# Performance work log

Hardware: AMD Instinct MI355X
Metric: run time of the kernel (lower is better)

The kernel has to match this reference:

```python
import jax, jax.numpy as jnp
import numpy as np

DIM = 128      # matrix dimension of the positional maps
N = 1024       # number of unique tree positions
MAX_POS = 65536  # positions < 2^16 -> path length <= 15 bits
L = 16         # static number of scan steps (covers max path length)


def setup_inputs() -> dict:
    key = jax.random.key(0)
    k1, k2 = jax.random.split(key)
    # replicate torch init: rand(2,d,d).softmax(-1).cumsum(-1)
    u = jax.random.uniform(k1, (2, DIM, DIM), dtype=jnp.float32)
    primitives = jnp.cumsum(jax.nn.softmax(u, axis=-1), axis=-1)
    unique = jax.random.randint(k2, (N,), 0, MAX_POS, dtype=jnp.int64)
    return {"unique": unique, "primitives": primitives}


def reference(unique, primitives):
    dtype = primitives.dtype
    dim = primitives.shape[-1]
    # hermitian = P - P^H (real -> skew-symmetric); primitives = matrix_exp(hermitian)
    herm = primitives - jnp.swapaxes(primitives, -1, -2)          # [2, d, d]
    expP = jax.vmap(jax.scipy.linalg.expm)(herm)                  # [2, d, d]
    eye = jnp.eye(dim, dtype=dtype)
    # linear(x, W) = x @ W.T ; word==2 (padding / exhausted path) applies identity
    trans = jnp.stack([expP[0].T, expP[1].T, eye])                # [3, d, d]

    # pos_to_path: bits of pos, LSB-first, dropping the leading 1.
    # bit at step s is (pos >> s) & 1, valid while (pos >> s) >= 2; pos<=1 -> empty path.
    steps = jnp.arange(L, dtype=unique.dtype)
    shifted = unique[None, :] >> steps[:, None]                   # [L, N]
    words = jnp.where(shifted >= 2, shifted & 1, 2)               # [L, N] in {0,1,2}

    def step(maps, w):
        # maps[n] <- maps[n] @ trans[w[n]]   (sequential composition along the path)
        return jnp.einsum('nij,njk->nik', maps, trans[w]), None

    maps0 = jnp.broadcast_to(eye, (unique.shape[0], dim, dim))    # identity.repeat(N,1,1)
    maps, _ = jax.lax.scan(step, maps0, words)
    return maps
```

## Files before the change

kernel.cpp:

```cpp
#include <hip/hip_runtime.h>

typedef unsigned int uint32;
typedef unsigned short u16;
typedef __attribute__((ext_vector_type(8))) short bf16x8;
typedef __attribute__((ext_vector_type(4))) float f32x4;
typedef __attribute__((ext_vector_type(2))) uint32 u32x2;
typedef __attribute__((ext_vector_type(4))) uint32 u32x4;

#define DIM 128
#define MAT (DIM * DIM)
#define GR  2048
#define PLANE 16384
#define MFMA __builtin_amdgcn_mfma_f32_16x16x32_bf16


__device__ __forceinline__ u16 f2bf(float x) {
    uint32 u = __float_as_uint(x);
    u += 0x7fffu + ((u >> 16) & 1u);
    return (u16)(u >> 16);
}
__device__ __forceinline__ float bf2f(u16 h) { return __uint_as_float(((uint32)h) << 16); }
__device__ __forceinline__ void split2(float x, u16& a0, u16& a1) {
    a0 = f2bf(x); a1 = f2bf(x - bf2f(a0));
}
__device__ __forceinline__ uint32 pack2(u16 a, u16 b) { return (uint32)a | ((uint32)b << 16); }
__device__ __forceinline__ uint4 packu4(const u16 (&a)[8]) {
    uint4 v; v.x = pack2(a[0], a[1]); v.y = pack2(a[2], a[3]);
    v.z = pack2(a[4], a[5]); v.w = pack2(a[6], a[7]); return v;
}
__device__ __forceinline__ uint32 comp4(const uint4& v, int c) {
    return c == 0 ? v.x : c == 1 ? v.y : c == 2 ? v.z : v.w;
}
__device__ __forceinline__ void transp8(const uint4 (&in)[8], uint4 (&out)[8]) {
#pragma unroll
    for (int c = 0; c < 8; ++c) {
        u16 o[8];
#pragma unroll
        for (int k = 0; k < 8; ++k) o[k] = (u16)(comp4(in[k], c >> 1) >> ((c & 1) * 16));
        out[c].x = pack2(o[0], o[1]); out[c].y = pack2(o[2], o[3]);
        out[c].z = pack2(o[4], o[5]); out[c].w = pack2(o[6], o[7]);
    }
}

template<bool PBLDS, int NP>
__device__ __forceinline__ void mm2(const uint4* __restrict__ pah, const uint4* __restrict__ pal,
                                    const uint4* __restrict__ pbh, const uint4* __restrict__ pbl,
                                    f32x4 (&acc)[4][4]) {
    const int tid = threadIdx.x, lane = tid & 63, w = tid >> 6;
    const int wr = (w >> 1) * 64, wc = (w & 1) * 64, lr = lane & 15, lg = lane >> 4;
#pragma unroll 1
    for (int kb = 0; kb < 4; ++kb) {
        const int g = kb * 4 + lg;
        bf16x8 ah[4], al[4], bh[4], bl[4];
#pragma unroll
        for (int t = 0; t < 4; ++t) {
            int ra = wr + t * 16 + lr;
            ah[t] = *(const bf16x8*)&pah[g * 128 + ra];
            if (NP == 3) al[t] = *(const bf16x8*)&pal[g * 128 + ra];
            int rb = wc + t * 16 + lr;
            int ib = PBLDS ? (rb * 16 + (g ^ (rb & 7))) : (g * 128 + rb);
            bh[t] = *(const bf16x8*)&pbh[ib];
            if (NP == 3) bl[t] = *(const bf16x8*)&pbl[ib];
        }
#pragma unroll
        for (int i = 0; i < 4; ++i)
#pragma unroll
            for (int j = 0; j < 4; ++j) {
                acc[i][j] = MFMA(ah[i], bh[j], acc[i][j], 0, 0, 0);
                if (NP == 3) {
                    acc[i][j] = MFMA(ah[i], bl[j], acc[i][j], 0, 0, 0);
                    acc[i][j] = MFMA(al[i], bh[j], acc[i][j], 0, 0, 0);
                }
            }
    }
}

__device__ __forceinline__ void acc_to_lds2(const f32x4 (&acc)[4][4], uint4* Mh, uint4* Ml) {
    const int tid = threadIdx.x, lane = tid & 63, w = tid >> 6;
    const int wr = (w >> 1) * 64, wc = (w & 1) * 64, lr = lane & 15, lg = lane >> 4;
#pragma unroll
    for (int i = 0; i < 4; ++i) {
        int u0 = wr + i * 16 + 4 * lg, half = (u0 >> 2) & 1, gq = u0 >> 3;
#pragma unroll
        for (int j = 0; j < 4; ++j) {
            int m = wc + j * 16 + lr;
            u16 h[4], l[4];
#pragma unroll
            for (int q = 0; q < 4; ++q) split2(acc[i][j][q], h[q], l[q]);
            uint2 hv; hv.x = pack2(h[0], h[1]); hv.y = pack2(h[2], h[3]);
            uint2 lv; lv.x = pack2(l[0], l[1]); lv.y = pack2(l[2], l[3]);
            int base = m * 16 + (gq ^ (m & 7));
            ((uint2*)&Mh[base])[half] = hv;
            ((uint2*)&Ml[base])[half] = lv;
        }
    }
}

__device__ __forceinline__ void acc_to_gN(const f32x4 (&acc)[4][4], uint4* nh, uint4* nl) {
    const int tid = threadIdx.x, lane = tid & 63, w = tid >> 6;
    const int wr = (w >> 1) * 64, wc = (w & 1) * 64, lr = lane & 15, lg = lane >> 4;
#pragma unroll
    for (int i = 0; i < 4; ++i) {
        int u0 = wr + i * 16 + 4 * lg, half = (u0 >> 2) & 1, gq = u0 >> 3;
#pragma unroll
        for (int j = 0; j < 4; ++j) {
            int m = wc + j * 16 + lr;
            u16 h[4], l[4];
#pragma unroll
            for (int q = 0; q < 4; ++q) split2(acc[i][j][q], h[q], l[q]);
            uint2 hv; hv.x = pack2(h[0], h[1]); hv.y = pack2(h[2], h[3]);
            uint2 lv; lv.x = pack2(l[0], l[1]); lv.y = pack2(l[2], l[3]);
            int base = gq * 128 + m;
            ((uint2*)&nh[base])[half] = hv;
            ((uint2*)&nl[base])[half] = lv;
        }
    }
}

__device__ __forceinline__ void acc_to_out(const f32x4 (&acc)[4][4], float* O) {
    const int tid = threadIdx.x, lane = tid & 63, w = tid >> 6;
    const int wr = (w >> 1) * 64, wc = (w & 1) * 64, lr = lane & 15, lg = lane >> 4;
#pragma unroll
    for (int i = 0; i < 4; ++i) {
        int u0 = wr + i * 16 + 4 * lg;
#pragma unroll
        for (int j = 0; j < 4; ++j) {
            int m = wc + j * 16 + lr;
            *(f32x4*)&O[m * DIM + u0] = acc[i][j];
        }
    }
}

__device__ __forceinline__ void stage_lds(const uint4* sh, const uint4* sl, uint4* Mh, uint4* Ml) {
    for (int s = threadIdx.x; s < GR; s += blockDim.x) {
        int g = s >> 7, row = s & 127;
        int d = row * 16 + (g ^ (row & 7));
        Mh[d] = sh[s]; Ml[d] = sl[s];
    }
}
__device__ __forceinline__ void copyN(const uint4* Mh, const uint4* Ml, uint4* dh, uint4* dl) {
    for (int s2 = threadIdx.x; s2 < 2 * GR; s2 += blockDim.x) {
        const uint4* src = (s2 & GR) ? Ml : Mh;
        uint4* dst = (s2 & GR) ? dl : dh;
        int s = s2 & (GR - 1);
        int g = s >> 7, row = s & 127;
        dst[s] = src[row * 16 + (g ^ (row & 7))];
    }
}
__device__ __forceinline__ void copyT(const uint4* Mh, const uint4* Ml, uint4* dh, uint4* dl) {
    for (int tk = threadIdx.x; tk < 512; tk += blockDim.x) {
        const uint4* src = (tk & 256) ? Ml : Mh;
        uint4* dst = (tk & 256) ? dl : dh;
        int t = tk & 255, br = t >> 4, bc = t & 15;
        uint4 in[8], out[8];
#pragma unroll
        for (int k = 0; k < 8; ++k) { int r = br * 8 + k; in[k] = src[r * 16 + (bc ^ (r & 7))]; }
        transp8(in, out);
#pragma unroll
        for (int k = 0; k < 8; ++k) dst[br * 128 + bc * 8 + k] = out[k];
    }
}


__device__ __forceinline__ void wlds2s(u16* dst, int m, int u0, f32x4 v) {
    u16 a0[4], a1[4];
#pragma unroll
    for (int q = 0; q < 4; ++q) split2(v[q], a0[q], a1[q]);
    int e = ((m >> 2) * 8 + (u0 >> 4)) * 64 + (m & 3) * 16 + (u0 & 15);
    uint2 w0; w0.x = pack2(a0[0], a0[1]); w0.y = pack2(a0[2], a0[3]);
    uint2 w1; w1.x = pack2(a1[0], a1[1]); w1.y = pack2(a1[2], a1[3]);
    *(uint2*)&dst[0 * PLANE + e] = w0;
    *(uint2*)&dst[1 * PLANE + e] = w1;
}

template<bool ATR>
__device__ __forceinline__ void mmS(const uint4* __restrict__ pa, const u16* __restrict__ XSu,
                                    f32x4 (&acc)[2][2], int wr, int wc, int lr, int lg) {
#pragma unroll
    for (int i = 0; i < 2; ++i)
#pragma unroll
        for (int j = 0; j < 2; ++j) { f32x4 z = {0.f, 0.f, 0.f, 0.f}; acc[i][j] = z; }
    const uint32 lds_base = (uint32)(size_t)(const void*)XSu;
#pragma unroll 1
    for (int kb = 0; kb < 4; ++kb) {
        const int g = kb * 4 + lg;
        u32x2 t0[2][2], t1[2][2];
        bf16x8 aa[2][2], bb[2][2];
        if (ATR) {
#pragma unroll
            for (int t = 0; t < 2; ++t) {
                uint32 ba = lds_base + (uint32)(((16 * g + (wr >> 4) + t) << 7) + 8 * lr);
#pragma unroll
                for (int sp = 0; sp < 2; ++sp) {
                    asm volatile("ds_read_b64_tr_b16 %0, %2\n\t"
                                 "ds_read_b64_tr_b16 %1, %2 offset:1024"
                                 : "=&v"(t0[t][sp]), "=&v"(t1[t][sp])
                                 : "v"(ba + (uint32)(sp * 2 * PLANE)));
                }
            }
        } else {
#pragma unroll
            for (int t = 0; t < 2; ++t) {
                int ra = wr + t * 16 + lr;
#pragma unroll
                for (int sp = 0; sp < 2; ++sp) aa[t][sp] = *(const bf16x8*)&pa[sp * GR + g * 128 + ra];
            }
        }
#pragma unroll
        for (int t = 0; t < 2; ++t) {
            int rb = wc + t * 16 + lr;
            int e = ((rb >> 2) * 8 + (g >> 1)) * 64 + (rb & 3) * 16 + (g & 1) * 8;
#pragma unroll
            for (int sp = 0; sp < 2; ++sp) bb[t][sp] = *(const bf16x8*)&XSu[sp * PLANE + e];
        }
        if (ATR) {
            asm volatile("s_waitcnt lgkmcnt(0)" ::: "memory");
            __builtin_amdgcn_sched_barrier(0);
#pragma unroll
            for (int t = 0; t < 2; ++t)
#pragma unroll
                for (int sp = 0; sp < 2; ++sp) {
                    u32x4 v; v.x = t0[t][sp].x; v.y = t0[t][sp].y;
                    v.z = t1[t][sp].x; v.w = t1[t][sp].y;
                    aa[t][sp] = *(bf16x8*)&v;
                }
        }
#pragma unroll
        for (int i = 0; i < 2; ++i)
#pragma unroll
            for (int j = 0; j < 2; ++j) {
                acc[i][j] = MFMA(aa[i][0], bb[j][0], acc[i][j], 0, 0, 0);
                acc[i][j] = MFMA(aa[i][0], bb[j][1], acc[i][j], 0, 0, 0);
                acc[i][j] = MFMA(aa[i][1], bb[j][0], acc[i][j], 0, 0, 0);
            }
    }
}

__global__ __launch_bounds__(1024) void expm_kernel(
        const float* __restrict__ P, float* __restrict__ NBf, float* __restrict__ NB2f,
        u16* TBp, u16* TB3p,
        u16* TThp, u16* TTlp, u16* TNhp, u16* TNlp) {
    __shared__ uint4 XL[4 * GR];
    u16* XSu = (u16*)XL;
    u16* PR0 = XSu;
    u16* PR1 = XSu + 2 * PLANE;
    const int b = blockIdx.x, tid = threadIdx.x;
    const int lane = tid & 63, w = tid >> 6;
    const int wr = (w >> 2) * 32, wc = (w & 3) * 32, lr = lane & 15, lg = lane >> 4;
    const float* Pm = P + b * MAT;
    float* nbf = NBf + b * MAT;
    float* nb2f = NB2f + b * MAT;
    uint4* tb  = (uint4*)TBp  + (size_t)b * 3 * GR;
    uint4* tb3 = (uint4*)TB3p + (size_t)b * 3 * GR;
    uint4* TTh = (uint4*)TThp; uint4* TTl = (uint4*)TTlp;
    uint4* TNh = (uint4*)TNhp; uint4* TNl = (uint4*)TNlp;

    const float C6f = 1.0f / 720.0f, C7f = 1.0f / 5040.0f, C8f = 1.0f / 40320.0f, C9f = 1.0f / 362880.0f;

    for (int s = tid; s < GR; s += 1024) {
        int r = s >> 4, g = s & 15;
        float vv[8];
#pragma unroll
        for (int k = 0; k < 8; ++k) {
            int c = g * 8 + k;
            vv[k] = (Pm[r * DIM + c] - Pm[c * DIM + r]) * (1.0f / 32.0f);
        }
        float4 f0; f0.x = vv[0]; f0.y = vv[1]; f0.z = vv[2]; f0.w = vv[3];
        float4 f1; f1.x = vv[4]; f1.y = vv[5]; f1.z = vv[6]; f1.w = vv[7];
        *(float4*)&nbf[r * DIM + g * 8] = f0;
        *(float4*)&nbf[r * DIM + g * 8 + 4] = f1;
        u16 s0[8], s1[8];
#pragma unroll
        for (int k = 0; k < 8; ++k) split2(vv[k], s0[k], s1[k]);
        int d = ((r >> 2) * 8 + (g >> 1)) * 64 + (r & 3) * 16 + (g & 1) * 8;
        *(uint4*)&PR0[0 * PLANE + d] = packu4(s0);
        *(uint4*)&PR0[1 * PLANE + d] = packu4(s1);
#pragma unroll
        for (int k = 0; k < 8; ++k) { s0[k] ^= 0x8000; s1[k] ^= 0x8000; }
        int gi = g * 128 + r;
        tb[0 * GR + gi] = packu4(s0); tb[1 * GR + gi] = packu4(s1);
    }
    __syncthreads();

    f32x4 acc[2][2];

    mmS<true>(nullptr, PR0, acc, wr, wc, lr, lg);
#pragma unroll
    for (int i = 0; i < 2; ++i) { int u0 = wr + i * 16 + 4 * lg;
#pragma unroll
        for (int j = 0; j < 2; ++j) { int m = wc + j * 16 + lr;
            *(f32x4*)&nb2f[m * DIM + u0] = acc[i][j];
            wlds2s(PR1, m, u0, acc[i][j]);
        } }
    __syncthreads();

    mmS<false>(tb, PR1, acc, wr, wc, lr, lg);
#pragma unroll
    for (int i = 0; i < 2; ++i) { int u0 = wr + i * 16 + 4 * lg; int half = (u0 >> 2) & 1; int gi = (u0 >> 3) * 128;
#pragma unroll
        for (int j = 0; j < 2; ++j) { int m = wc + j * 16 + lr;
            f32x4 a = acc[i][j];
            u16 a0[4], a1[4];
#pragma unroll
            for (int q = 0; q < 4; ++q) split2(-a[q], a0[q], a1[q]);
            uint2 w0; w0.x = pack2(a0[0], a0[1]); w0.y = pack2(a0[2], a0[3]);
            uint2 w1; w1.x = pack2(a1[0], a1[1]); w1.y = pack2(a1[2], a1[3]);
            ((uint2*)&tb3[0 * GR + gi + m])[half] = w0;
            ((uint2*)&tb3[1 * GR + gi + m])[half] = w1;
            f32x4 bv = *(const f32x4*)&nbf[m * DIM + u0];
            f32x4 b2v = *(const f32x4*)&nb2f[m * DIM + u0];
            f32x4 x0;
#pragma unroll
            for (int q = 0; q < 4; ++q)
                x0[q] = a[q] * C9f + b2v[q] * C8f + bv[q] * C7f + ((u0 + q == m) ? C6f : 0.0f);
            wlds2s(PR0, m, u0, x0);
        } }
    __syncthreads();

    mmS<false>(tb3, PR0, acc, wr, wc, lr, lg);
#pragma unroll
    for (int i = 0; i < 2; ++i) { int u0 = wr + i * 16 + 4 * lg;
#pragma unroll
        for (int j = 0; j < 2; ++j) { int m = wc + j * 16 + lr;
            f32x4 bv = *(const f32x4*)&nbf[m * DIM + u0];
            f32x4 b2v = *(const f32x4*)&nb2f[m * DIM + u0];
            f32x4 x1;
#pragma unroll
            for (int q = 0; q < 4; ++q)
                x1[q] = acc[i][j][q] + bv[q] * (1.0f / 24.0f) + b2v[q] * (1.0f / 120.0f)
                      + ((u0 + q == m) ? (1.0f / 6.0f) : 0.0f);
            wlds2s(PR1, m, u0, x1);
        } }
    __syncthreads();

    mmS<false>(tb3, PR1, acc, wr, wc, lr, lg);
#pragma unroll
    for (int i = 0; i < 2; ++i) { int u0 = wr + i * 16 + 4 * lg;
#pragma unroll
        for (int j = 0; j < 2; ++j) { int m = wc + j * 16 + lr;
            f32x4 bv = *(const f32x4*)&nbf[m * DIM + u0];
            f32x4 b2v = *(const f32x4*)&nb2f[m * DIM + u0];
            f32x4 x2;
#pragma unroll
            for (int q = 0; q < 4; ++q)
                x2[q] = acc[i][j][q] + bv[q] + b2v[q] * 0.5f + ((u0 + q == m) ? 1.0f : 0.0f);
            wlds2s(PR0, m, u0, x2);
        } }
    __syncthreads();

    for (int sq = 0; sq < 5; ++sq) {
        const u16* src = (sq & 1) ? PR1 : PR0;
        u16* dst = (sq & 1) ? PR0 : PR1;
        mmS<true>(nullptr, src, acc, wr, wc, lr, lg);
        if (sq < 4) {
#pragma unroll
            for (int i = 0; i < 2; ++i) { int u0 = wr + i * 16 + 4 * lg;
#pragma unroll
                for (int j = 0; j < 2; ++j) wlds2s(dst, wc + j * 16 + lr, u0, acc[i][j]);
            }
            __syncthreads();
        } else {
#pragma unroll
            for (int i = 0; i < 2; ++i) { int u0 = wr + i * 16 + 4 * lg; int half = (u0 >> 2) & 1;
#pragma unroll
                for (int j = 0; j < 2; ++j) { int m = wc + j * 16 + lr;
                    u16 h[4], l[4];
#pragma unroll
                    for (int q = 0; q < 4; ++q) split2(acc[i][j][q], h[q], l[q]);
                    uint2 hv; hv.x = pack2(h[0], h[1]); hv.y = pack2(h[2], h[3]);
                    uint2 lv; lv.x = pack2(l[0], l[1]); lv.y = pack2(l[2], l[3]);
                    int base = m * 16 + ((u0 >> 3) ^ (m & 7));
                    ((uint2*)&XL[2 * GR + base])[half] = hv;
                    ((uint2*)&XL[3 * GR + base])[half] = lv;
                } }
            __syncthreads();
            copyN(XL + 2 * GR, XL + 3 * GR, TTh + (size_t)b * GR, TTl + (size_t)b * GR);
            copyT(XL + 2 * GR, XL + 3 * GR, TNh + (size_t)b * GR, TNl + (size_t)b * GR);
        }
    }
}

__global__ __launch_bounds__(256) void chain_kernel(u16* TThp, u16* TTlp, u16* TNhp, u16* TNlp,
                                                    int schemeA) {
    __shared__ uint4 Mh[GR], Ml[GR];
    uint4* TTh = (uint4*)TThp; uint4* TTl = (uint4*)TTlp;
    uint4* TNh = (uint4*)TNhp; uint4* TNl = (uint4*)TNlp;
    int b = blockIdx.x;
    if (b == 28) {
        int id = schemeA ? 274 : 126;
        for (int s = threadIdx.x; s < GR; s += 256) {
            int g = s >> 7, row = s & 127;
            u16 h[8];
#pragma unroll
            for (int k = 0; k < 8; ++k) h[k] = (g * 8 + k == row) ? (u16)0x3F80 : (u16)0;
            TNh[(size_t)id * GR + s] = packu4(h);
            uint4 z; z.x = z.y = z.z = z.w = 0u;
            TNl[(size_t)id * GR + s] = z;
        }
        return;
    }
    int v = 4 + b;
    int nb = 31 - __clz(v);
    int b0 = v & 1;
    stage_lds(TNh + (size_t)b0 * GR, TNl + (size_t)b0 * GR, Mh, Ml);
    __syncthreads();
    for (int t = 1; t < nb; ++t) {
        int bt = (v >> t) & 1;
        f32x4 acc[4][4] = {};
        mm2<true, 3>(TTh + (size_t)bt * GR, TTl + (size_t)bt * GR, Mh, Ml, acc);
        __syncthreads();
        acc_to_lds2(acc, Mh, Ml);
        __syncthreads();
    }
    copyT(Mh, Ml, TTh + (size_t)(v - 2) * GR, TTl + (size_t)(v - 2) * GR);
    bool needN = schemeA ? (v >= 16) : true;
    if (needN) {
        int tn = schemeA ? (v - 14) : (v - 2);
        copyN(Mh, Ml, TNh + (size_t)tn * GR, TNl + (size_t)tn * GR);
    }
}

__global__ __launch_bounds__(256) void pair_kernel(u16* TThp, u16* TTlp, u16* TNhp, u16* TNlp,
                                                   int schemeA) {
    extern __shared__ uint4 PL[];
    uint4* TTh = (uint4*)TThp; uint4* TTl = (uint4*)TTlp;
    uint4* TNh = (uint4*)TNhp; uint4* TNl = (uint4*)TNlp;
    int v = 32 + blockIdx.x;
    int c4 = v & 15;
    int tnb = schemeA ? (2 + c4) : (14 + c4);
    int tta = (v >> 4) - 2;
    if (schemeA) {
        f32x4 acc[4][4] = {};
        if (v < 256) {
            mm2<false, 3>(TNh + (size_t)tnb * GR, TNl + (size_t)tnb * GR,
                          TTh + (size_t)tta * GR, TTl + (size_t)tta * GR, acc);
            acc_to_gN(acc, TTh + (size_t)(v - 2) * GR, TTl + (size_t)(v - 2) * GR);
        } else {
            mm2<false, 3>(TTh + (size_t)tta * GR, TTl + (size_t)tta * GR,
                          TNh + (size_t)tnb * GR, TNl + (size_t)tnb * GR, acc);
            int tn = 18 + (v - 256);
            acc_to_gN(acc, TNh + (size_t)tn * GR, TNl + (size_t)tn * GR);
        }
    } else {
        f32x4 acc[4][4] = {};
        mm2<false, 3>(TTh + (size_t)tta * GR, TTl + (size_t)tta * GR,
                      TNh + (size_t)tnb * GR, TNl + (size_t)tnb * GR, acc);
        acc_to_gN(acc, TNh + (size_t)(v - 2) * GR, TNl + (size_t)(v - 2) * GR);
        acc_to_lds2(acc, PL, PL + GR);
        __syncthreads();
        copyT(PL, PL + GR, TTh + (size_t)(v - 2) * GR, TTl + (size_t)(v - 2) * GR);
    }
}

__global__ __launch_bounds__(256) void final_kernel(const u16* TThp, const u16* TTlp,
                                                    const u16* TNhp, const u16* TNlp,
                                                    const int* __restrict__ uq,
                                                    float* __restrict__ out, int schemeA) {
    extern __shared__ uint4 FL[];
    const uint4* TTh = (const uint4*)TThp; const uint4* TTl = (const uint4*)TTlp;
    const uint4* TNh = (const uint4*)TNhp; const uint4* TNl = (const uint4*)TNlp;
    float* O = out + (size_t)blockIdx.x * MAT;
    unsigned p = (unsigned)uq[blockIdx.x];

    if (p < 2u) {
        for (int s = threadIdx.x; s < 4096; s += 256) {
            int r = s >> 5, c0 = (s & 31) * 4;
            float4 v; v.x = v.y = v.z = v.w = 0.f;
            int d = r - c0;
            if (d == 0) v.x = 1.f; else if (d == 1) v.y = 1.f;
            else if (d == 2) v.z = 1.f; else if (d == 3) v.w = 1.f;
            *(float4*)&O[r * DIM + c0] = v;
        }
        return;
    }

    const uint4 *pah, *pal, *pbh, *pbl;
    int m3 = -1;
    if (schemeA) {
        const int id = 274;
        if (p < 256u) {
            pah = TTh + (size_t)(p - 2) * GR; pal = TTl + (size_t)(p - 2) * GR;
            pbh = TNh + (size_t)id * GR;      pbl = TNl + (size_t)id * GR;
        } else {
            int lo = (int)(p & 255u); unsigned hi = p >> 8;
            pbh = TNh + (size_t)(18 + lo) * GR; pbl = TNl + (size_t)(18 + lo) * GR;
            if (hi >= 2u) { pah = TTh + (size_t)(hi - 2) * GR; pal = TTl + (size_t)(hi - 2) * GR; }
            else          { pah = TNh + (size_t)id * GR;       pal = TNl + (size_t)id * GR; }
        }
        f32x4 acc[4][4] = {};
        mm2<false, 1>(pah, pal, pbh, pbl, acc);
        acc_to_out(acc, O);
        return;
    }
    {
        int f[3]; int m = 0; unsigned q = p;
        while (q >= 128u) { f[m++] = 64 + (int)(q & 63u); q >>= 6; }
        f[m++] = (int)q;
        if (m == 1) {
            const uint4* sh = TNh + (size_t)(f[0] - 2) * GR;
            const uint4* sl = TNl + (size_t)(f[0] - 2) * GR;
            for (int s = threadIdx.x; s < GR; s += 256) {
                int row = s >> 4, g = s & 15;
                uint4 H = sh[g * 128 + row], L = sl[g * 128 + row];
                float4 o0, o1;
                o0.x = bf2f((u16)(H.x & 0xffff)) + bf2f((u16)(L.x & 0xffff));
                o0.y = bf2f((u16)(H.x >> 16))    + bf2f((u16)(L.x >> 16));
                o0.z = bf2f((u16)(H.y & 0xffff)) + bf2f((u16)(L.y & 0xffff));
                o0.w = bf2f((u16)(H.y >> 16))    + bf2f((u16)(L.y >> 16));
                o1.x = bf2f((u16)(H.z & 0xffff)) + bf2f((u16)(L.z & 0xffff));
                o1.y = bf2f((u16)(H.z >> 16))    + bf2f((u16)(L.z >> 16));
                o1.z = bf2f((u16)(H.w & 0xffff)) + bf2f((u16)(L.w & 0xffff));
                o1.w = bf2f((u16)(H.w >> 16))    + bf2f((u16)(L.w >> 16));
                *(float4*)&O[row * DIM + g * 8] = o0;
                *(float4*)&O[row * DIM + g * 8 + 4] = o1;
            }
            return;
        }
        pbh = TNh + (size_t)(f[0] - 2) * GR; pbl = TNl + (size_t)(f[0] - 2) * GR;
        pah = TTh + (size_t)(f[1] - 2) * GR; pal = TTl + (size_t)(f[1] - 2) * GR;
        if (m == 3) m3 = f[2] - 2;
    }

    f32x4 acc[4][4] = {};
    mm2<false, 3>(pah, pal, pbh, pbl, acc);
    if (m3 < 0) { acc_to_out(acc, O); return; }
    acc_to_lds2(acc, FL, FL + GR);
    __syncthreads();
    f32x4 a2[4][4] = {};
    mm2<true, 3>(TTh + (size_t)m3 * GR, TTl + (size_t)m3 * GR, FL, FL + GR, a2);
    acc_to_out(a2, O);
}

extern "C" void kernel_launch(void* const* d_in, const int* in_sizes, int n_in,
                              void* d_out, int out_size, void* d_ws, size_t ws_size,
                              hipStream_t stream) {
    const int*   uq = (const int*)d_in[0];
    const float* P  = (const float*)d_in[1];
    float* out = (float*)d_out;

    const size_t needA = (size_t)(2 * 254 + 2 * 275 + 18) * MAT * 2 + (size_t)4 * MAT * 4;
    const bool A = ws_size >= needA;
    const int nTT = A ? 254 : 126;
    const int nTN = A ? 275 : 127;

    u16* TTh = (u16*)d_ws;
    u16* TTl = TTh + (size_t)nTT * MAT;
    u16* TNh = TTl + (size_t)nTT * MAT;
    u16* TNl = TNh + (size_t)nTN * MAT;
    u16* TB  = TNl + (size_t)nTN * MAT;
    u16* TB3 = TB  + (size_t)6 * MAT;
    u16* XTg = TB3 + (size_t)6 * MAT;
    float* NBf  = (float*)(XTg + (size_t)6 * MAT);
    float* NB2f = NBf + 2 * MAT;

    expm_kernel<<<2, 1024, 0, stream>>>(P, NBf, NB2f, TB, TB3, TTh, TTl, TNh, TNl);
    chain_kernel<<<29, 256, 0, stream>>>(TTh, TTl, TNh, TNl, (int)A);
    pair_kernel<<<A ? 480 : 96, 256, A ? 0 : 65536, stream>>>(TTh, TTl, TNh, TNl, (int)A);
    final_kernel<<<1024, 256, A ? 0 : 65536, stream>>>(TTh, TTl, TNh, TNl, uq, out, (int)A);
}
```

Measured before the change: 112.1 us.

## Rebalance thread counts: 512-thread expm with wider tiles, 1024-thread chain

The expm kernel drops from 1024 to 512 threads, so each wave computes a 32x64 tile (2x4 MFMA tiles) instead of 32x32. This gives more reuse of each A fragment and needs fewer waves to synchronise. The chain kernel goes from 256 to 1024 threads with a new 16-wave matmul (mm2w) and writeback (acc_to_lds2w). Each wave now owns a 32x32 tile, which spreads the serial chain of matrix products over more waves and shortens each one. In exchange, expm has fewer waves to hide latency and uses more registers per thread, and chain pays for more barrier participants.

```diff
diff --git a/kernel.cpp b/kernel.cpp
--- a/kernel.cpp
+++ b/kernel.cpp
@@ -131,6 +131,56 @@
     }
 }
 
+__device__ __forceinline__ void mm2w(const uint4* __restrict__ pah, const uint4* __restrict__ pal,
+                                     const uint4* __restrict__ pbh, const uint4* __restrict__ pbl,
+                                     f32x4 (&acc)[2][2]) {
+    const int tid = threadIdx.x, lane = tid & 63, w = tid >> 6;
+    const int wr = (w >> 2) * 32, wc = (w & 3) * 32, lr = lane & 15, lg = lane >> 4;
+#pragma unroll 1
+    for (int kb = 0; kb < 4; ++kb) {
+        const int g = kb * 4 + lg;
+        bf16x8 ah[2], al[2], bh[2], bl[2];
+#pragma unroll
+        for (int t = 0; t < 2; ++t) {
+            int ra = wr + t * 16 + lr;
+            ah[t] = *(const bf16x8*)&pah[g * 128 + ra];
+            al[t] = *(const bf16x8*)&pal[g * 128 + ra];
+            int rb = wc + t * 16 + lr;
+            int ib = rb * 16 + (g ^ (rb & 7));
+            bh[t] = *(const bf16x8*)&pbh[ib];
+            bl[t] = *(const bf16x8*)&pbl[ib];
+        }
+#pragma unroll
+        for (int i = 0; i < 2; ++i)
+#pragma unroll
+            for (int j = 0; j < 2; ++j) {
+                acc[i][j] = MFMA(ah[i], bh[j], acc[i][j], 0, 0, 0);
+                acc[i][j] = MFMA(ah[i], bl[j], acc[i][j], 0, 0, 0);
+                acc[i][j] = MFMA(al[i], bh[j], acc[i][j], 0, 0, 0);
+            }
+    }
+}
+__device__ __forceinline__ void acc_to_lds2w(const f32x4 (&acc)[2][2], uint4* Mh, uint4* Ml) {
+    const int tid = threadIdx.x, lane = tid & 63, w = tid >> 6;
+    const int wr = (w >> 2) * 32, wc = (w & 3) * 32, lr = lane & 15, lg = lane >> 4;
+#pragma unroll
+    for (int i = 0; i < 2; ++i) {
+        int u0 = wr + i * 16 + 4 * lg, half = (u0 >> 2) & 1, gq = u0 >> 3;
+#pragma unroll
+        for (int j = 0; j < 2; ++j) {
+            int m = wc + j * 16 + lr;
+            u16 h[4], l[4];
+#pragma unroll
+            for (int q = 0; q < 4; ++q) split2(acc[i][j][q], h[q], l[q]);
+            uint2 hv; hv.x = pack2(h[0], h[1]); hv.y = pack2(h[2], h[3]);
+            uint2 lv; lv.x = pack2(l[0], l[1]); lv.y = pack2(l[2], l[3]);
+            int base = m * 16 + (gq ^ (m & 7));
+            ((uint2*)&Mh[base])[half] = hv;
+            ((uint2*)&Ml[base])[half] = lv;
+        }
+    }
+}
+
 __device__ __forceinline__ void stage_lds(const uint4* sh, const uint4* sl, uint4* Mh, uint4* Ml) {
     for (int s = threadIdx.x; s < GR; s += blockDim.x) {
         int g = s >> 7, row = s & 127;
@@ -175,17 +225,17 @@
 
 template<bool ATR>
 __device__ __forceinline__ void mmS(const uint4* __restrict__ pa, const u16* __restrict__ XSu,
-                                    f32x4 (&acc)[2][2], int wr, int wc, int lr, int lg) {
+                                    f32x4 (&acc)[2][4], int wr, int wc, int lr, int lg) {
 #pragma unroll
     for (int i = 0; i < 2; ++i)
 #pragma unroll
-        for (int j = 0; j < 2; ++j) { f32x4 z = {0.f, 0.f, 0.f, 0.f}; acc[i][j] = z; }
+        for (int j = 0; j < 4; ++j) { f32x4 z = {0.f, 0.f, 0.f, 0.f}; acc[i][j] = z; }
     const uint32 lds_base = (uint32)(size_t)(const void*)XSu;
 #pragma unroll 1
     for (int kb = 0; kb < 4; ++kb) {
         const int g = kb * 4 + lg;
         u32x2 t0[2][2], t1[2][2];
-        bf16x8 aa[2][2], bb[2][2];
+        bf16x8 aa[2][2], bb[4][2];
         if (ATR) {
 #pragma unroll
             for (int t = 0; t < 2; ++t) {
@@ -207,7 +257,7 @@
             }
         }
 #pragma unroll
-        for (int t = 0; t < 2; ++t) {
+        for (int t = 0; t < 4; ++t) {
             int rb = wc + t * 16 + lr;
             int e = ((rb >> 2) * 8 + (g >> 1)) * 64 + (rb & 3) * 16 + (g & 1) * 8;
 #pragma unroll
@@ -228,7 +278,7 @@
 #pragma unroll
         for (int i = 0; i < 2; ++i)
 #pragma unroll
-            for (int j = 0; j < 2; ++j) {
+            for (int j = 0; j < 4; ++j) {
                 acc[i][j] = MFMA(aa[i][0], bb[j][0], acc[i][j], 0, 0, 0);
                 acc[i][j] = MFMA(aa[i][0], bb[j][1], acc[i][j], 0, 0, 0);
                 acc[i][j] = MFMA(aa[i][1], bb[j][0], acc[i][j], 0, 0, 0);
@@ -236,7 +286,7 @@
     }
 }
 
-__global__ __launch_bounds__(1024) void expm_kernel(
+__global__ __launch_bounds__(512) void expm_kernel(
         const float* __restrict__ P, float* __restrict__ NBf, float* __restrict__ NB2f,
         u16* TBp, u16* TB3p,
         u16* TThp, u16* TTlp, u16* TNhp, u16* TNlp) {
@@ -246,7 +296,7 @@
     u16* PR1 = XSu + 2 * PLANE;
     const int b = blockIdx.x, tid = threadIdx.x;
     const int lane = tid & 63, w = tid >> 6;
-    const int wr = (w >> 2) * 32, wc = (w & 3) * 32, lr = lane & 15, lg = lane >> 4;
+    const int wr = (w >> 1) * 32, wc = (w & 1) * 64, lr = lane & 15, lg = lane >> 4;
     const float* Pm = P + b * MAT;
     float* nbf = NBf + b * MAT;
     float* nb2f = NB2f + b * MAT;
@@ -257,7 +307,7 @@
 
     const float C6f = 1.0f / 720.0f, C7f = 1.0f / 5040.0f, C8f = 1.0f / 40320.0f, C9f = 1.0f / 362880.0f;
 
-    for (int s = tid; s < GR; s += 1024) {
+    for (int s = tid; s < GR; s += 512) {
         int r = s >> 4, g = s & 15;
         float vv[8];
 #pragma unroll
@@ -282,13 +332,13 @@
     }
     __syncthreads();
 
-    f32x4 acc[2][2];
+    f32x4 acc[2][4];
 
     mmS<true>(nullptr, PR0, acc, wr, wc, lr, lg);
 #pragma unroll
     for (int i = 0; i < 2; ++i) { int u0 = wr + i * 16 + 4 * lg;
 #pragma unroll
-        for (int j = 0; j < 2; ++j) { int m = wc + j * 16 + lr;
+        for (int j = 0; j < 4; ++j) { int m = wc + j * 16 + lr;
             *(f32x4*)&nb2f[m * DIM + u0] = acc[i][j];
             wlds2s(PR1, m, u0, acc[i][j]);
         } }
@@ -298,7 +348,7 @@
 #pragma unroll
     for (int i = 0; i < 2; ++i) { int u0 = wr + i * 16 + 4 * lg; int half = (u0 >> 2) & 1; int gi = (u0 >> 3) * 128;
 #pragma unroll
-        for (int j = 0; j < 2; ++j) { int m = wc + j * 16 + lr;
+        for (int j = 0; j < 4; ++j) { int m = wc + j * 16 + lr;
             f32x4 a = acc[i][j];
             u16 a0[4], a1[4];
 #pragma unroll
@@ -321,7 +371,7 @@
 #pragma unroll
     for (int i = 0; i < 2; ++i) { int u0 = wr + i * 16 + 4 * lg;
 #pragma unroll
-        for (int j = 0; j < 2; ++j) { int m = wc + j * 16 + lr;
+        for (int j = 0; j < 4; ++j) { int m = wc + j * 16 + lr;
             f32x4 bv = *(const f32x4*)&nbf[m * DIM + u0];
             f32x4 b2v = *(const f32x4*)&nb2f[m * DIM + u0];
             f32x4 x1;
@@ -337,7 +387,7 @@
 #pragma unroll
     for (int i = 0; i < 2; ++i) { int u0 = wr + i * 16 + 4 * lg;
 #pragma unroll
-        for (int j = 0; j < 2; ++j) { int m = wc + j * 16 + lr;
+        for (int j = 0; j < 4; ++j) { int m = wc + j * 16 + lr;
             f32x4 bv = *(const f32x4*)&nbf[m * DIM + u0];
             f32x4 b2v = *(const f32x4*)&nb2f[m * DIM + u0];
             f32x4 x2;
@@ -356,14 +406,14 @@
 #pragma unroll
             for (int i = 0; i < 2; ++i) { int u0 = wr + i * 16 + 4 * lg;
 #pragma unroll
-                for (int j = 0; j < 2; ++j) wlds2s(dst, wc + j * 16 + lr, u0, acc[i][j]);
+                for (int j = 0; j < 4; ++j) wlds2s(dst, wc + j * 16 + lr, u0, acc[i][j]);
             }
             __syncthreads();
         } else {
 #pragma unroll
             for (int i = 0; i < 2; ++i) { int u0 = wr + i * 16 + 4 * lg; int half = (u0 >> 2) & 1;
 #pragma unroll
-                for (int j = 0; j < 2; ++j) { int m = wc + j * 16 + lr;
+                for (int j = 0; j < 4; ++j) { int m = wc + j * 16 + lr;
                     u16 h[4], l[4];
 #pragma unroll
                     for (int q = 0; q < 4; ++q) split2(acc[i][j][q], h[q], l[q]);
@@ -380,15 +430,15 @@
     }
 }
 
-__global__ __launch_bounds__(256) void chain_kernel(u16* TThp, u16* TTlp, u16* TNhp, u16* TNlp,
-                                                    int schemeA) {
+__global__ __launch_bounds__(1024) void chain_kernel(u16* TThp, u16* TTlp, u16* TNhp, u16* TNlp,
+                                                     int schemeA) {
     __shared__ uint4 Mh[GR], Ml[GR];
     uint4* TTh = (uint4*)TThp; uint4* TTl = (uint4*)TTlp;
     uint4* TNh = (uint4*)TNhp; uint4* TNl = (uint4*)TNlp;
     int b = blockIdx.x;
     if (b == 28) {
         int id = schemeA ? 274 : 126;
-        for (int s = threadIdx.x; s < GR; s += 256) {
+        for (int s = threadIdx.x; s < GR; s += 1024) {
             int g = s >> 7, row = s & 127;
             u16 h[8];
 #pragma unroll
@@ -406,10 +456,10 @@
     __syncthreads();
     for (int t = 1; t < nb; ++t) {
         int bt = (v >> t) & 1;
-        f32x4 acc[4][4] = {};
-        mm2<true, 3>(TTh + (size_t)bt * GR, TTl + (size_t)bt * GR, Mh, Ml, acc);
+        f32x4 acc[2][2] = {};
+        mm2w(TTh + (size_t)bt * GR, TTl + (size_t)bt * GR, Mh, Ml, acc);
         __syncthreads();
-        acc_to_lds2(acc, Mh, Ml);
+        acc_to_lds2w(acc, Mh, Ml);
         __syncthreads();
     }
     copyT(Mh, Ml, TTh + (size_t)(v - 2) * GR, TTl + (size_t)(v - 2) * GR);
@@ -553,8 +603,8 @@
     float* NBf  = (float*)(XTg + (size_t)6 * MAT);
     float* NB2f = NBf + 2 * MAT;
 
-    expm_kernel<<<2, 1024, 0, stream>>>(P, NBf, NB2f, TB, TB3, TTh, TTl, TNh, TNl);
-    chain_kernel<<<29, 256, 0, stream>>>(TTh, TTl, TNh, TNl, (int)A);
+    expm_kernel<<<2, 512, 0, stream>>>(P, NBf, NB2f, TB, TB3, TTh, TTl, TNh, TNl);
+    chain_kernel<<<29, 1024, 0, stream>>>(TTh, TTl, TNh, TNl, (int)A);
     pair_kernel<<<A ? 480 : 96, 256, A ? 0 : 65536, stream>>>(TTh, TTl, TNh, TNl, (int)A);
     final_kernel<<<1024, 256, A ? 0 : 65536, stream>>>(TTh, TTl, TNh, TNl, uq, out, (int)A);
 }
```

After: 104.1 us. -7.1%, faster.
